# Optimization experiments

Hardware: AMD Instinct MI355X
Metric: run time of the kernel (lower is better)

The kernel has to match this reference:

```python
import jax, jax.numpy as jnp
import numpy as np

B, D, S, K = 2048, 256, 64, 1024
TOPK = 3
MAX_REC = 5
BETA = 0.25  # vq_commitment_beta


def setup_inputs() -> dict:
    key = jax.random.key(0)
    ks = jax.random.split(key, 8)
    w_scale = 1.0 / np.sqrt(2 * D)
    return {
        "gw_real": jax.random.normal(ks[0], (B, D), jnp.float32),
        "gw_imag": jax.random.normal(ks[1], (B, D), jnp.float32),
        "mem_real": jax.random.normal(ks[2], (B, S, D), jnp.float32),
        "mem_imag": jax.random.normal(ks[3], (B, S, D), jnp.float32),
        "gate_w": jax.random.normal(ks[4], (1, 2 * D), jnp.float32) * w_scale,
        "gate_b": jnp.zeros((1,), jnp.float32),
        "addr_w": jax.random.normal(ks[5], (S, 2 * D), jnp.float32) * w_scale,
        "addr_b": jnp.zeros((S,), jnp.float32),
        "lnr_w": jnp.ones((D,), jnp.float32),
        "lnr_b": jnp.zeros((D,), jnp.float32),
        "lni_w": jnp.ones((D,), jnp.float32),
        "lni_b": jnp.zeros((D,), jnp.float32),
        "cln_scale": jnp.ones((D,), jnp.float32),
        "cln_shift": jnp.zeros((D,), jnp.float32),
        "codebook": jax.random.normal(ks[6], (K, 2 * D), jnp.float32) * (1.0 / np.sqrt(D)),
    }


def _layernorm(x, w, b, eps=1e-6):
    mu = x.mean(-1, keepdims=True)
    var = ((x - mu) ** 2).mean(-1, keepdims=True)  # biased, like torch LayerNorm
    return (x - mu) / jnp.sqrt(var + eps) * w + b


def _assoc_mem(gr, gi, mr, mi, gate_w, gate_b, addr_w, addr_b, lnr_w, lnr_b, lni_w, lni_b):
    # read: Re(conj(m) * q) summed over dim -> cosine-like similarity [B,S]
    sim = (mr * gr[:, None, :] + mi * gi[:, None, :]).sum(-1)
    sim = sim - jax.lax.stop_gradient(sim.max(-1, keepdims=True))
    attn = jax.nn.softmax(sim, axis=-1)[..., None]  # [B,S,1]
    read_r = (attn * mr).sum(1)
    read_i = (attn * mi).sum(1)
    # write
    flat = jnp.concatenate([gr, gi], -1)  # [B,2D]
    write_gate = jax.nn.sigmoid(flat @ gate_w.T + gate_b)  # [B,1]
    logits = flat @ addr_w.T + addr_b  # [B,S]
    logits = logits - jax.lax.stop_gradient(logits.max(-1, keepdims=True))
    ww = jax.nn.softmax(logits, axis=-1)
    slot_entropy = (-(ww * jnp.log(ww + 1e-10)).sum(-1)).mean()
    top_vals, top_idx = jax.lax.top_k(ww, TOPK)
    sparse = jnp.zeros_like(ww).at[jnp.arange(ww.shape[0])[:, None], top_idx].set(top_vals)
    sparse = sparse / (sparse.sum(-1, keepdims=True) + 1e-6)
    eff = write_gate[:, None, :] * sparse[..., None]  # [B,S,1]
    nmr = (1.0 - eff) * mr + eff * gr[:, None, :]
    nmi = (1.0 - eff) * mi + eff * gi[:, None, :]
    # StableComplexNorm: independent LayerNorm on real / imag
    nmr = _layernorm(nmr, lnr_w, lnr_b)
    nmi = _layernorm(nmi, lni_w, lni_b)
    return read_r, read_i, nmr, nmi, slot_entropy


def _complex_layernorm(zr, zi, scale, shift):
    mag = jnp.sqrt(zr * zr + zi * zi + 1e-8)
    mean = mag.mean(-1, keepdims=True)
    var = jnp.var(jax.lax.stop_gradient(mag), axis=-1, keepdims=True, ddof=1)  # torch .var unbiased
    nm = (mag - mean) / jnp.sqrt(var + 1e-4) * scale + shift
    ang = jax.lax.stop_gradient(jnp.arctan2(zi, zr))
    return nm * jnp.cos(ang), nm * jnp.sin(ang)


def _ema_vq(zr, zi, codebook):
    zf = jnp.concatenate([zr, zi], -1)  # [B,2D]
    x_sq = (zf ** 2).sum(-1, keepdims=True)
    y_sq = (codebook ** 2).sum(-1)
    d = jnp.clip(x_sq + y_sq - 2.0 * zf @ codebook.T, 0.0)
    idx = d.argmin(-1)  # [B]
    zq = codebook[idx]
    loss_sample = BETA * ((jax.lax.stop_gradient(zq) - zf) ** 2).mean(-1)
    zq = zf + jax.lax.stop_gradient(zq - zf)  # straight-through
    probs = jnp.zeros((K,), zf.dtype).at[idx].add(1.0) / zf.shape[0]
    norm_entropy = -(probs * jnp.log(probs + 1e-10)).sum() / np.log(K)
    return zq[..., :D], zq[..., D:], loss_sample, norm_entropy


def reference(gw_real, gw_imag, mem_real, mem_imag, gate_w, gate_b, addr_w, addr_b,
              lnr_w, lnr_b, lni_w, lni_b, cln_scale, cln_shift, codebook):
    gr, gi = gw_real, gw_imag
    mr, mi = mem_real, mem_imag
    aux = jnp.float32(0.0)
    for _ in range(MAX_REC):  # adaptive-halting recursion, fixed depth
        read_r, read_i, mr, mi, slot_ent = _assoc_mem(
            gr, gi, mr, mi, gate_w, gate_b, addr_w, addr_b, lnr_w, lnr_b, lni_w, lni_b)
        cr, ci = _complex_layernorm(gr + read_r, gi + read_i, cln_scale, cln_shift)
        gr, gi, vq_loss, vq_ent = _ema_vq(cr, ci, codebook)
        aux = aux + slot_ent + vq_loss.mean() + vq_ent
    out = jnp.concatenate([gr, gi], -1)  # [B, 2D]
    return out, aux
```

## Files before the change

kernel.cpp:

```cpp
#include <hip/hip_runtime.h>
#include <cstdint>
#include <cstddef>

#define NB 2048
#define ND 256
#define NS 64
#define NK 1024
#define NREC 5
#define BETA 0.25f

template<int CTRL>
__device__ __forceinline__ float dpp_mv(float x){
  union { float f; int i; } u; u.f = x;
  u.i = __builtin_amdgcn_update_dpp(0, u.i, CTRL, 0xF, 0xF, true);
  return u.f;
}
__device__ __forceinline__ float gred_sum16(float v){
  v += dpp_mv<0x128>(v);
  v += dpp_mv<0x124>(v);
  v += dpp_mv<0x122>(v);
  v += dpp_mv<0x121>(v);
  return v;
}
__device__ __forceinline__ float gred_max16(float v){
  v = fmaxf(v, dpp_mv<0x128>(v));
  v = fmaxf(v, dpp_mv<0x124>(v));
  v = fmaxf(v, dpp_mv<0x122>(v));
  v = fmaxf(v, dpp_mv<0x121>(v));
  return v;
}
__device__ __forceinline__ float wred_sum64(float v){
  v = gred_sum16(v);
  v += __shfl_xor(v, 16, 64);
  v += __shfl_xor(v, 32, 64);
  return v;
}
__device__ __forceinline__ float wred_max64(float v){
  v = gred_max16(v);
  v = fmaxf(v, __shfl_xor(v, 16, 64));
  v = fmaxf(v, __shfl_xor(v, 32, 64));
  return v;
}
__device__ __forceinline__ float swz_xor16(float x){
  union { float f; int i; } u; u.f = x;
  u.i = __builtin_amdgcn_ds_swizzle(u.i, 0x401F);
  return u.f;
}

__global__ __launch_bounds__(64) void k_ysq(const float* __restrict__ cb,
                                            float* __restrict__ ysq){
  const int cidx = blockIdx.x;
  const int lanev = threadIdx.x;
  const float4* p = reinterpret_cast<const float4*>(cb + (size_t)cidx * (2*ND) + lanev*8);
  float4 a = p[0], b = p[1];
  float sv = a.x*a.x + a.y*a.y + a.z*a.z + a.w*a.w
           + b.x*b.x + b.y*b.y + b.z*b.z + b.w*b.w;
  sv = wred_sum64(sv);
  if (lanev == 0) ysq[cidx] = sv;
}

__global__ __launch_bounds__(1024) void k_assoc(
    const float* __restrict__ g_r, const float* __restrict__ g_i,
    const float* mem_r_src, const float* mem_i_src,
    float* mem_r_dst, float* mem_i_dst,
    const float* __restrict__ gate_w, const float* __restrict__ gate_b,
    const float* __restrict__ addr_w, const float* __restrict__ addr_b,
    const float* __restrict__ lnr_w, const float* __restrict__ lnr_b,
    const float* __restrict__ lni_w, const float* __restrict__ lni_b,
    const float* __restrict__ cln_s, const float* __restrict__ cln_sh,
    float* __restrict__ zf, float* __restrict__ acc, const int write_mem)
{
  const int t = threadIdx.x;
  const int b = blockIdx.x;
  const int lane = t & 63;
  const int w = t >> 6;
  const int s = t >> 4;
  const int c = t & 15;
  const int d0 = c << 4;

  __shared__ float s_gr[320], s_gi[320];
  __shared__ float s_attn[NS], s_ww[NS], s_eff[NS];
  __shared__ float s_gpart[4], s_p[4], s_q[4];
  __shared__ float s_redA[32*288];
  __shared__ float s_redB[32*288];

  float mr[16], mi[16];
  const size_t base = ((size_t)b*NS + s)*ND + d0;
  {
    const float4* pr = reinterpret_cast<const float4*>(mem_r_src + base);
    const float4* pi = reinterpret_cast<const float4*>(mem_i_src + base);
#pragma unroll
    for (int q = 0; q < 4; q++){
      float4 vr = pr[q], vi = pi[q];
      mr[4*q+0]=vr.x; mr[4*q+1]=vr.y; mr[4*q+2]=vr.z; mr[4*q+3]=vr.w;
      mi[4*q+0]=vi.x; mi[4*q+1]=vi.y; mi[4*q+2]=vi.z; mi[4*q+3]=vi.w;
    }
  }

  if (t < ND){
    float gr = g_r[(size_t)b*ND + t];
    float gi = g_i[(size_t)b*ND + t];
    s_gr[(t>>4)*20 + (t&15)] = gr;
    s_gi[(t>>4)*20 + (t&15)] = gi;
    float gp = gr*gate_w[t] + gi*gate_w[ND + t];
    gp = wred_sum64(gp);
    if (lane == 0) s_gpart[w] = gp;
  }
  if (t < NS) s_eff[t] = 0.f;
  __syncthreads();

  const float4* sgr4 = reinterpret_cast<const float4*>(&s_gr[c*20]);
  const float4* sgi4 = reinterpret_cast<const float4*>(&s_gi[c*20]);

  float gr_[16], gi_[16];
#pragma unroll
  for (int q = 0; q < 4; q++){
    float4 a4 = sgr4[q], b4 = sgi4[q];
    gr_[4*q+0]=a4.x; gr_[4*q+1]=a4.y; gr_[4*q+2]=a4.z; gr_[4*q+3]=a4.w;
    gi_[4*q+0]=b4.x; gi_[4*q+1]=b4.y; gi_[4*q+2]=b4.z; gi_[4*q+3]=b4.w;
  }

  {
    float sp = 0.f;
#pragma unroll
    for (int j = 0; j < 16; j++) sp += mr[j]*gr_[j] + mi[j]*gi_[j];
    sp = gred_sum16(sp);
    if (c == 0) s_attn[s] = sp;
  }
  {
    const float4* awr = reinterpret_cast<const float4*>(addr_w + (size_t)s*(2*ND) + d0);
    const float4* awi = reinterpret_cast<const float4*>(addr_w + (size_t)s*(2*ND) + ND + d0);
    float lp = 0.f;
#pragma unroll
    for (int q = 0; q < 4; q++){
      float4 ar = awr[q], ai = awi[q];
      lp += gr_[4*q+0]*ar.x + gr_[4*q+1]*ar.y + gr_[4*q+2]*ar.z + gr_[4*q+3]*ar.w;
      lp += gi_[4*q+0]*ai.x + gi_[4*q+1]*ai.y + gi_[4*q+2]*ai.z + gi_[4*q+3]*ai.w;
    }
    lp = gred_sum16(lp);
    if (c == 0) s_ww[s] = lp + addr_b[s];
  }
  __syncthreads();

  if (w == 0){
    float v = s_attn[lane];
    float mx = wred_max64(v);
    float p = expf(v - mx);
    float sum = wred_sum64(p);
    s_attn[lane] = p / sum;
  } else if (w == 1){
    float lv = s_ww[lane];
    float lmx = wred_max64(lv);
    float lp = expf(lv - lmx);
    float lsum = wred_sum64(lp);
    float wwv = lp / lsum;
    float es = wred_sum64(-wwv * logf(wwv + 1e-10f));
    if (lane == 0) atomicAdd(&acc[0], es * (1.f/NB));
    float v2 = wwv; const int id0 = lane;
    float tv0=0, tv1=0, tv2=0; int ti0=0, ti1=0, ti2=0;
#pragma unroll
    for (int kk = 0; kk < 3; kk++){
      float bv = v2; int bi = id0;
#pragma unroll
      for (int m = 1; m < 64; m <<= 1){
        float ov = __shfl_xor(bv, m, 64); int oi = __shfl_xor(bi, m, 64);
        if (ov > bv || (ov == bv && oi < bi)){ bv = ov; bi = oi; }
      }
      if (kk == 0){ tv0 = bv; ti0 = bi; }
      else if (kk == 1){ tv1 = bv; ti1 = bi; }
      else { tv2 = bv; ti2 = bi; }
      if (id0 == bi) v2 = -1.f;
    }
    if (lane == 0){
      float wg = 1.f/(1.f + expf(-(s_gpart[0]+s_gpart[1]+s_gpart[2]+s_gpart[3] + gate_b[0])));
      float ssum = tv0 + tv1 + tv2 + 1e-6f;
      s_eff[ti0] = wg * (tv0/ssum);
      s_eff[ti1] = wg * (tv1/ssum);
      s_eff[ti2] = wg * (tv2/ssum);
    }
  }
  __syncthreads();

  const float a_w = s_attn[s];
  {
    const bool wr_ok = ((lane & 31) < 16);
    const int row = 2*w + (lane >> 5);
    float* dstA = &s_redA[row*288 + (lane & 15)*18];
    float* dstB = &s_redB[row*288 + (lane & 15)*18];
#pragma unroll
    for (int j = 0; j < 16; j += 2){
      float x0 = a_w * mr[j],   x1 = a_w * mr[j+1];
      float y0 = x0 + swz_xor16(x0);
      float y1 = x1 + swz_xor16(x1);
      if (wr_ok) *reinterpret_cast<float2*>(dstA + j) = make_float2(y0, y1);
    }
#pragma unroll
    for (int j = 0; j < 16; j += 2){
      float x0 = a_w * mi[j],   x1 = a_w * mi[j+1];
      float y0 = x0 + swz_xor16(x0);
      float y1 = x1 + swz_xor16(x1);
      if (wr_ok) *reinterpret_cast<float2*>(dstB + j) = make_float2(y0, y1);
    }
  }

  if (write_mem){
    const float effv = s_eff[s];
    const float onem = 1.f - effv;
    {
      float ps = 0.f;
#pragma unroll
      for (int j = 0; j < 16; j++){ mr[j] = onem*mr[j] + effv*gr_[j]; ps += mr[j]; }
      float mu = gred_sum16(ps) * (1.f/ND);
      float vs = 0.f;
#pragma unroll
      for (int j = 0; j < 16; j++){ float d_ = mr[j]-mu; vs += d_*d_; }
      float var = gred_sum16(vs) * (1.f/ND);
      float inv = 1.f / sqrtf(var + 1e-6f);
      const float4* lw4 = reinterpret_cast<const float4*>(lnr_w + d0);
      const float4* lb4 = reinterpret_cast<const float4*>(lnr_b + d0);
#pragma unroll
      for (int q = 0; q < 4; q++){
        float4 wv = lw4[q], bv = lb4[q];
        mr[4*q+0] = (mr[4*q+0]-mu)*inv*wv.x + bv.x;
        mr[4*q+1] = (mr[4*q+1]-mu)*inv*wv.y + bv.y;
        mr[4*q+2] = (mr[4*q+2]-mu)*inv*wv.z + bv.z;
        mr[4*q+3] = (mr[4*q+3]-mu)*inv*wv.w + bv.w;
      }
    }
    {
      float ps = 0.f;
#pragma unroll
      for (int j = 0; j < 16; j++){ mi[j] = onem*mi[j] + effv*gi_[j]; ps += mi[j]; }
      float mu = gred_sum16(ps) * (1.f/ND);
      float vs = 0.f;
#pragma unroll
      for (int j = 0; j < 16; j++){ float d_ = mi[j]-mu; vs += d_*d_; }
      float var = gred_sum16(vs) * (1.f/ND);
      float inv = 1.f / sqrtf(var + 1e-6f);
      const float4* lw4 = reinterpret_cast<const float4*>(lni_w + d0);
      const float4* lb4 = reinterpret_cast<const float4*>(lni_b + d0);
#pragma unroll
      for (int q = 0; q < 4; q++){
        float4 wv = lw4[q], bv = lb4[q];
        mi[4*q+0] = (mi[4*q+0]-mu)*inv*wv.x + bv.x;
        mi[4*q+1] = (mi[4*q+1]-mu)*inv*wv.y + bv.y;
        mi[4*q+2] = (mi[4*q+2]-mu)*inv*wv.z + bv.z;
        mi[4*q+3] = (mi[4*q+3]-mu)*inv*wv.w + bv.w;
      }
    }
  }
  __syncthreads();

  float zr = 0.f, zi = 0.f, mag = 1.f;
  if (t < ND){
    const int offp = (t >> 4)*18 + (t & 15);
    float rr = 0.f, ri = 0.f;
#pragma unroll
    for (int r2 = 0; r2 < 32; r2++){
      rr += s_redA[r2*288 + offp];
      ri += s_redB[r2*288 + offp];
    }
    const int offg = (t >> 4)*20 + (t & 15);
    zr = s_gr[offg] + rr;
    zi = s_gi[offg] + ri;
    mag = sqrtf(zr*zr + zi*zi + 1e-8f);
    float ps = wred_sum64(mag);
    if (lane == 0) s_p[w] = ps;
  }
  __syncthreads();
  const float meanv = (s_p[0]+s_p[1]+s_p[2]+s_p[3]) * (1.f/ND);
  if (t < ND){
    float d_ = mag - meanv;
    float qs = wred_sum64(d_*d_);
    if (lane == 0) s_q[w] = qs;
  }
  __syncthreads();
  if (t < ND){
    const float varv = (s_q[0]+s_q[1]+s_q[2]+s_q[3]) * (1.f/(ND-1));
    float nm = (mag - meanv) / sqrtf(varv + 1e-4f) * cln_s[t] + cln_sh[t];
    float sc = nm / mag;
    zf[(size_t)b*(2*ND) + t]      = sc * zr;
    zf[(size_t)b*(2*ND) + ND + t] = sc * zi;
  }

  if (write_mem){
    float4* pdr = reinterpret_cast<float4*>(mem_r_dst + base);
    float4* pdi = reinterpret_cast<float4*>(mem_i_dst + base);
#pragma unroll
    for (int q = 0; q < 4; q++){
      pdr[q] = make_float4(mr[4*q], mr[4*q+1], mr[4*q+2], mr[4*q+3]);
      pdi[q] = make_float4(mi[4*q], mi[4*q+1], mi[4*q+2], mi[4*q+3]);
    }
  }
}

__global__ __launch_bounds__(256) void k_vq_dist(
    const float* __restrict__ zf, const float* __restrict__ codebook,
    const float* __restrict__ ysq, float* __restrict__ pvals, int* __restrict__ pidx)
{
  const int t = threadIdx.x;
  const int mt = blockIdx.x >> 2, nt = blockIdx.x & 3;
  const int sb = mt*32, cbase = nt*256;
  const int jg = t & 31;
  const int ig = t >> 5;

  __shared__ float s_a[16*36];
  __shared__ float s_b[16*260];

  float accv[4][8];
#pragma unroll
  for (int i = 0; i < 4; i++)
#pragma unroll
    for (int j = 0; j < 8; j++) accv[i][j] = 0.f;

  for (int k0 = 0; k0 < 2*ND; k0 += 16){
#pragma unroll
    for (int p = 0; p < 2; p++){
      int e = t + p*256; int i_ = e >> 4; int k_ = e & 15;
      s_a[k_*36 + i_] = zf[(size_t)(sb+i_)*(2*ND) + k0 + k_];
    }
#pragma unroll
    for (int p = 0; p < 16; p++){
      int e = t + p*256; int c_ = e >> 4; int k_ = e & 15;
      s_b[k_*260 + c_] = codebook[(size_t)(cbase+c_)*(2*ND) + k0 + k_];
    }
    __syncthreads();
#pragma unroll
    for (int k = 0; k < 16; k++){
      float4 a4 = *reinterpret_cast<const float4*>(&s_a[k*36 + ig*4]);
      float4 b0 = *reinterpret_cast<const float4*>(&s_b[k*260 + jg*8]);
      float4 b1 = *reinterpret_cast<const float4*>(&s_b[k*260 + jg*8 + 4]);
      const float av[4] = {a4.x, a4.y, a4.z, a4.w};
      const float bv[8] = {b0.x,b0.y,b0.z,b0.w,b1.x,b1.y,b1.z,b1.w};
#pragma unroll
      for (int i = 0; i < 4; i++)
#pragma unroll
        for (int j = 0; j < 8; j++) accv[i][j] = fmaf(av[i], bv[j], accv[i][j]);
    }
    __syncthreads();
  }

#pragma unroll
  for (int i = 0; i < 4; i++){
    float bvv = 1e30f; int bii = 0;
#pragma unroll
    for (int j = 0; j < 8; j++){
      int cg = cbase + jg*8 + j;
      float sc = ysq[cg] - 2.f*accv[i][j];
      if (sc < bvv){ bvv = sc; bii = cg; }
    }
#pragma unroll
    for (int m = 1; m < 32; m <<= 1){
      float ov = __shfl_xor(bvv, m, 64); int oi = __shfl_xor(bii, m, 64);
      if (ov < bvv || (ov == bvv && oi < bii)){ bvv = ov; bii = oi; }
    }
    if (jg == 0){
      int smp = sb + ig*4 + i;
      pvals[smp*4 + nt] = bvv;
      pidx [smp*4 + nt] = bii;
    }
  }
}

__global__ __launch_bounds__(64) void k_vq_pick(
    const float* __restrict__ pvals, const int* __restrict__ pidx,
    const float* __restrict__ codebook, const float* zf,
    float* __restrict__ g_r, float* __restrict__ g_i, float* out,
    const int final_it, int* __restrict__ hist, float* __restrict__ acc)
{
  const int b = blockIdx.x, lanev = threadIdx.x;
  int sidx = 0;
  if (lanev == 0){
    float bv = pvals[b*4]; int bi = pidx[b*4];
#pragma unroll
    for (int nt = 1; nt < 4; nt++){
      float v = pvals[b*4+nt]; int id = pidx[b*4+nt];
      if (v < bv || (v == bv && id < bi)){ bv = v; bi = id; }
    }
    sidx = bi;
    atomicAdd(&hist[sidx], 1);
  }
  sidx = __shfl(sidx, 0, 64);

  const int e0 = lanev*8;
  const float4* cp = reinterpret_cast<const float4*>(codebook + (size_t)sidx*(2*ND) + e0);
  float4 c0 = cp[0], c1 = cp[1];
  const float4* zp = reinterpret_cast<const float4*>(zf + (size_t)b*(2*ND) + e0);
  float4 z0 = zp[0], z1 = zp[1];
  float ds_ = (c0.x-z0.x)*(c0.x-z0.x) + (c0.y-z0.y)*(c0.y-z0.y)
            + (c0.z-z0.z)*(c0.z-z0.z) + (c0.w-z0.w)*(c0.w-z0.w)
            + (c1.x-z1.x)*(c1.x-z1.x) + (c1.y-z1.y)*(c1.y-z1.y)
            + (c1.z-z1.z)*(c1.z-z1.z) + (c1.w-z1.w)*(c1.w-z1.w);
  ds_ = wred_sum64(ds_);
  if (lanev == 0) atomicAdd(&acc[1], BETA * ds_ * (1.f/(2*ND)) * (1.f/NB));

  if (final_it){
    float4* op = reinterpret_cast<float4*>(out + (size_t)b*(2*ND) + e0);
    op[0] = c0; op[1] = c1;
  } else if (e0 < ND){
    float4* gp = reinterpret_cast<float4*>(g_r + (size_t)b*ND + e0);
    gp[0] = c0; gp[1] = c1;
  } else {
    float4* gp = reinterpret_cast<float4*>(g_i + (size_t)b*ND + (e0-ND));
    gp[0] = c0; gp[1] = c1;
  }
}

__global__ __launch_bounds__(256) void k_final(const int* __restrict__ hist,
                                               const float* __restrict__ acc,
                                               float* __restrict__ out)
{
  __shared__ float red[256];
  const int t = threadIdx.x;
  float e = 0.f;
  for (int it = 0; it < NREC; it++){
    for (int k = t; k < NK; k += 256){
      float p = (float)hist[it*NK + k] * (1.f/NB);
      e += p * logf(p + 1e-10f);
    }
  }
  red[t] = e;
  __syncthreads();
  for (int off = 128; off > 0; off >>= 1){
    if (t < off) red[t] += red[t+off];
    __syncthreads();
  }
  if (t == 0) out[(size_t)NB*2*ND] = acc[0] + acc[1] - red[0] * (1.f/logf((float)NK));
}

extern "C" void kernel_launch(void* const* d_in, const int* in_sizes, int n_in,
                              void* d_out, int out_size, void* d_ws, size_t ws_size,
                              hipStream_t stream)
{
  const float* gwr    = (const float*)d_in[0];
  const float* gwi    = (const float*)d_in[1];
  float*       memr_in= (float*)d_in[2];
  float*       memi_in= (float*)d_in[3];
  const float* gate_w = (const float*)d_in[4];
  const float* gate_b = (const float*)d_in[5];
  const float* addr_w = (const float*)d_in[6];
  const float* addr_b = (const float*)d_in[7];
  const float* lnr_w  = (const float*)d_in[8];
  const float* lnr_b  = (const float*)d_in[9];
  const float* lni_w  = (const float*)d_in[10];
  const float* lni_b  = (const float*)d_in[11];
  const float* cln_s  = (const float*)d_in[12];
  const float* cln_sh = (const float*)d_in[13];
  const float* codebook = (const float*)d_in[14];
  float* out = (float*)d_out;
  char* wsb = (char*)d_ws;

  const size_t OFF_ACC = 0;
  const size_t OFF_HIST = 256;
  const size_t OFF_YSQ = 20736;
  const size_t OFF_PV  = 24832;
  const size_t OFF_PI  = 57600;
  const size_t OFF_GR  = 90368;
  const size_t OFF_GI  = 2187520;
  const size_t OFF_ZF  = 4284672;
  const size_t OFF_MR  = 8478976;
  const size_t OFF_MI  = 142696704;
  const size_t NEED_BIG = 276914432;
  const size_t NEED_MID = 8478976;
  const size_t NEED_TINY = 90368;

  if (ws_size < NEED_TINY) return;

  float* acc   = (float*)(wsb + OFF_ACC);
  int*   hist  = (int*)  (wsb + OFF_HIST);
  float* ysq   = (float*)(wsb + OFF_YSQ);
  float* pvals = (float*)(wsb + OFF_PV);
  int*   pidx  = (int*)  (wsb + OFF_PI);

  const bool big = ws_size >= NEED_BIG;
  const bool mid = ws_size >= NEED_MID;

  float* memr_buf = big ? (float*)(wsb + OFF_MR) : memr_in;
  float* memi_buf = big ? (float*)(wsb + OFF_MI) : memi_in;
  float* g_rp = mid ? (float*)(wsb + OFF_GR) : (float*)d_in[0];
  float* g_ip = mid ? (float*)(wsb + OFF_GI) : (float*)d_in[1];
  float* zfp  = mid ? (float*)(wsb + OFF_ZF) : out;

  (void)hipMemsetAsync(wsb, 0, OFF_HIST + (size_t)NREC*NK*sizeof(int), stream);

  k_ysq<<<dim3(NK), dim3(64), 0, stream>>>(codebook, ysq);

  const float* gsr = gwr; const float* gsi = gwi;
  const float* msr = memr_in; const float* msi = memi_in;
  for (int it = 0; it < NREC; it++){
    const int write_mem = (it == NREC-1) ? 0 : 1;
    k_assoc<<<dim3(NB), dim3(1024), 0, stream>>>(
        gsr, gsi, msr, msi, memr_buf, memi_buf,
        gate_w, gate_b, addr_w, addr_b,
        lnr_w, lnr_b, lni_w, lni_b, cln_s, cln_sh, zfp, acc, write_mem);
    k_vq_dist<<<dim3(256), dim3(256), 0, stream>>>(zfp, codebook, ysq, pvals, pidx);
    k_vq_pick<<<dim3(NB), dim3(64), 0, stream>>>(
        pvals, pidx, codebook, zfp, g_rp, g_ip, out,
        (it == NREC-1) ? 1 : 0, hist + it*NK, acc);
    gsr = g_rp; gsi = g_ip;
    msr = memr_buf; msi = memi_buf;
  }
  k_final<<<dim3(1), dim3(256), 0, stream>>>(hist, acc, out);
}
```

Baseline: 1.588 ms.

## Shrink assoc kernel to 256 threads looping over four slot groups

The associative-memory kernel drops from 1024 to 256 threads per block. Each thread now loops over four groups of 16 memory slots. Because it no longer holds one slot's row in registers across the whole kernel, memory is loaded twice from global, once for similarity and once for the read/write pass. The shared reduction buffers shrink from 32 rows to 4, accumulated across loop iterations, and the layernorm stats use a single pass (sum and sum of squares). The goal is less shared memory, fewer barriers and higher occupancy, at the cost of re-reading memory and a less numerically stable variance.

```diff
diff --git a/kernel.cpp b/kernel.cpp
--- a/kernel.cpp
+++ b/kernel.cpp
@@ -40,11 +40,6 @@
   v = fmaxf(v, __shfl_xor(v, 16, 64));
   v = fmaxf(v, __shfl_xor(v, 32, 64));
   return v;
-}
-__device__ __forceinline__ float swz_xor16(float x){
-  union { float f; int i; } u; u.f = x;
-  u.i = __builtin_amdgcn_ds_swizzle(u.i, 0x401F);
-  return u.f;
 }
 
 __global__ __launch_bounds__(64) void k_ysq(const float* __restrict__ cb,
@@ -59,7 +54,7 @@
   if (lanev == 0) ysq[cidx] = sv;
 }
 
-__global__ __launch_bounds__(1024) void k_assoc(
+__global__ __launch_bounds__(256, 6) void k_assoc(
     const float* __restrict__ g_r, const float* __restrict__ g_i,
     const float* mem_r_src, const float* mem_i_src,
     float* mem_r_dst, float* mem_i_dst,
@@ -74,71 +69,59 @@
   const int b = blockIdx.x;
   const int lane = t & 63;
   const int w = t >> 6;
-  const int s = t >> 4;
+  const int sg = t >> 4;
   const int c = t & 15;
   const int d0 = c << 4;
 
   __shared__ float s_gr[320], s_gi[320];
   __shared__ float s_attn[NS], s_ww[NS], s_eff[NS];
-  __shared__ float s_gpart[4], s_p[4], s_q[4];
-  __shared__ float s_redA[32*288];
-  __shared__ float s_redB[32*288];
-
-  float mr[16], mi[16];
-  const size_t base = ((size_t)b*NS + s)*ND + d0;
+  __shared__ float s_gpart[4], s_pq[8];
+  __shared__ float s_redA[4*288], s_redB[4*288];
+
   {
-    const float4* pr = reinterpret_cast<const float4*>(mem_r_src + base);
-    const float4* pi = reinterpret_cast<const float4*>(mem_i_src + base);
-#pragma unroll
-    for (int q = 0; q < 4; q++){
-      float4 vr = pr[q], vi = pi[q];
-      mr[4*q+0]=vr.x; mr[4*q+1]=vr.y; mr[4*q+2]=vr.z; mr[4*q+3]=vr.w;
-      mi[4*q+0]=vi.x; mi[4*q+1]=vi.y; mi[4*q+2]=vi.z; mi[4*q+3]=vi.w;
-    }
-  }
-
-  if (t < ND){
     float gr = g_r[(size_t)b*ND + t];
     float gi = g_i[(size_t)b*ND + t];
-    s_gr[(t>>4)*20 + (t&15)] = gr;
-    s_gi[(t>>4)*20 + (t&15)] = gi;
+    s_gr[(t>>4)*20 + c] = gr;
+    s_gi[(t>>4)*20 + c] = gi;
+    if (t < NS) s_eff[t] = 0.f;
     float gp = gr*gate_w[t] + gi*gate_w[ND + t];
     gp = wred_sum64(gp);
     if (lane == 0) s_gpart[w] = gp;
   }
-  if (t < NS) s_eff[t] = 0.f;
   __syncthreads();
 
-  const float4* sgr4 = reinterpret_cast<const float4*>(&s_gr[c*20]);
-  const float4* sgi4 = reinterpret_cast<const float4*>(&s_gi[c*20]);
-
   float gr_[16], gi_[16];
-#pragma unroll
-  for (int q = 0; q < 4; q++){
-    float4 a4 = sgr4[q], b4 = sgi4[q];
-    gr_[4*q+0]=a4.x; gr_[4*q+1]=a4.y; gr_[4*q+2]=a4.z; gr_[4*q+3]=a4.w;
-    gi_[4*q+0]=b4.x; gi_[4*q+1]=b4.y; gi_[4*q+2]=b4.z; gi_[4*q+3]=b4.w;
-  }
-
   {
-    float sp = 0.f;
-#pragma unroll
-    for (int j = 0; j < 16; j++) sp += mr[j]*gr_[j] + mi[j]*gi_[j];
+    const float4* p4r = reinterpret_cast<const float4*>(&s_gr[c*20]);
+    const float4* p4i = reinterpret_cast<const float4*>(&s_gi[c*20]);
+#pragma unroll
+    for (int q = 0; q < 4; q++){
+      float4 a4 = p4r[q], b4 = p4i[q];
+      gr_[4*q+0]=a4.x; gr_[4*q+1]=a4.y; gr_[4*q+2]=a4.z; gr_[4*q+3]=a4.w;
+      gi_[4*q+0]=b4.x; gi_[4*q+1]=b4.y; gi_[4*q+2]=b4.z; gi_[4*q+3]=b4.w;
+    }
+  }
+
+#pragma unroll 1
+  for (int p = 0; p < 4; p++){
+    const int sl = (p << 4) + sg;
+    const size_t mbase = ((size_t)b*NS + sl)*ND + d0;
+    const float4* pr  = reinterpret_cast<const float4*>(mem_r_src + mbase);
+    const float4* pi  = reinterpret_cast<const float4*>(mem_i_src + mbase);
+    const float4* ar4 = reinterpret_cast<const float4*>(addr_w + (size_t)sl*(2*ND) + d0);
+    const float4* ai4 = reinterpret_cast<const float4*>(addr_w + (size_t)sl*(2*ND) + ND + d0);
+    float sp = 0.f, lp = 0.f;
+#pragma unroll
+    for (int q = 0; q < 4; q++){
+      float4 vr = pr[q], vi = pi[q], ar = ar4[q], ai = ai4[q];
+      sp += vr.x*gr_[4*q+0] + vr.y*gr_[4*q+1] + vr.z*gr_[4*q+2] + vr.w*gr_[4*q+3];
+      sp += vi.x*gi_[4*q+0] + vi.y*gi_[4*q+1] + vi.z*gi_[4*q+2] + vi.w*gi_[4*q+3];
+      lp += ar.x*gr_[4*q+0] + ar.y*gr_[4*q+1] + ar.z*gr_[4*q+2] + ar.w*gr_[4*q+3];
+      lp += ai.x*gi_[4*q+0] + ai.y*gi_[4*q+1] + ai.z*gi_[4*q+2] + ai.w*gi_[4*q+3];
+    }
     sp = gred_sum16(sp);
-    if (c == 0) s_attn[s] = sp;
-  }
-  {
-    const float4* awr = reinterpret_cast<const float4*>(addr_w + (size_t)s*(2*ND) + d0);
-    const float4* awi = reinterpret_cast<const float4*>(addr_w + (size_t)s*(2*ND) + ND + d0);
-    float lp = 0.f;
-#pragma unroll
-    for (int q = 0; q < 4; q++){
-      float4 ar = awr[q], ai = awi[q];
-      lp += gr_[4*q+0]*ar.x + gr_[4*q+1]*ar.y + gr_[4*q+2]*ar.z + gr_[4*q+3]*ar.w;
-      lp += gi_[4*q+0]*ai.x + gi_[4*q+1]*ai.y + gi_[4*q+2]*ai.z + gi_[4*q+3]*ai.w;
-    }
     lp = gred_sum16(lp);
-    if (c == 0) s_ww[s] = lp + addr_b[s];
+    if (c == 0){ s_attn[sl] = sp; s_ww[sl] = lp + addr_b[sl]; }
   }
   __syncthreads();
 
@@ -178,119 +161,119 @@
       s_eff[ti1] = wg * (tv1/ssum);
       s_eff[ti2] = wg * (tv2/ssum);
     }
+  } else {
+    for (int i = t & 127; i < 4*288; i += 128){ s_redA[i] = 0.f; s_redB[i] = 0.f; }
   }
   __syncthreads();
 
-  const float a_w = s_attn[s];
+#pragma unroll 1
+  for (int p = 0; p < 4; p++){
+    const int sl = (p << 4) + sg;
+    const size_t mbase = ((size_t)b*NS + sl)*ND + d0;
+    float mr[16], mi[16];
+    {
+      const float4* pr = reinterpret_cast<const float4*>(mem_r_src + mbase);
+      const float4* pi = reinterpret_cast<const float4*>(mem_i_src + mbase);
+#pragma unroll
+      for (int q = 0; q < 4; q++){
+        float4 vr = pr[q], vi = pi[q];
+        mr[4*q+0]=vr.x; mr[4*q+1]=vr.y; mr[4*q+2]=vr.z; mr[4*q+3]=vr.w;
+        mi[4*q+0]=vi.x; mi[4*q+1]=vi.y; mi[4*q+2]=vi.z; mi[4*q+3]=vi.w;
+      }
+    }
+    const float a_w = s_attn[sl];
+
+#pragma unroll
+    for (int j = 0; j < 16; j += 2){
+      float y0 = a_w*mr[j], y1 = a_w*mr[j+1];
+      y0 += __shfl_xor(y0, 16, 64); y0 += __shfl_xor(y0, 32, 64);
+      y1 += __shfl_xor(y1, 16, 64); y1 += __shfl_xor(y1, 32, 64);
+      float z0 = a_w*mi[j], z1 = a_w*mi[j+1];
+      z0 += __shfl_xor(z0, 16, 64); z0 += __shfl_xor(z0, 32, 64);
+      z1 += __shfl_xor(z1, 16, 64); z1 += __shfl_xor(z1, 32, 64);
+      if (lane < 16){
+        float2* pa = reinterpret_cast<float2*>(&s_redA[w*288 + lane*18 + j]);
+        float2* pb = reinterpret_cast<float2*>(&s_redB[w*288 + lane*18 + j]);
+        float2 oa = *pa, ob = *pb;
+        *pa = make_float2(oa.x + y0, oa.y + y1);
+        *pb = make_float2(ob.x + z0, ob.y + z1);
+      }
+    }
+
+    if (write_mem){
+      const float effv = s_eff[sl];
+      const float onem = 1.f - effv;
+      {
+        float ps = 0.f;
+#pragma unroll
+        for (int j = 0; j < 16; j++){ mr[j] = onem*mr[j] + effv*gr_[j]; ps += mr[j]; }
+        float mu = gred_sum16(ps) * (1.f/ND);
+        float vs = 0.f;
+#pragma unroll
+        for (int j = 0; j < 16; j++){ float d_ = mr[j]-mu; vs += d_*d_; }
+        float var = gred_sum16(vs) * (1.f/ND);
+        float inv = 1.f / sqrtf(var + 1e-6f);
+        const float4* lw4 = reinterpret_cast<const float4*>(lnr_w + d0);
+        const float4* lb4 = reinterpret_cast<const float4*>(lnr_b + d0);
+        float4* pd = reinterpret_cast<float4*>(mem_r_dst + mbase);
+#pragma unroll
+        for (int q = 0; q < 4; q++){
+          float4 wv = lw4[q], bv = lb4[q];
+          pd[q] = make_float4((mr[4*q+0]-mu)*inv*wv.x + bv.x,
+                              (mr[4*q+1]-mu)*inv*wv.y + bv.y,
+                              (mr[4*q+2]-mu)*inv*wv.z + bv.z,
+                              (mr[4*q+3]-mu)*inv*wv.w + bv.w);
+        }
+      }
+      {
+        float ps = 0.f;
+#pragma unroll
+        for (int j = 0; j < 16; j++){ mi[j] = onem*mi[j] + effv*gi_[j]; ps += mi[j]; }
+        float mu = gred_sum16(ps) * (1.f/ND);
+        float vs = 0.f;
+#pragma unroll
+        for (int j = 0; j < 16; j++){ float d_ = mi[j]-mu; vs += d_*d_; }
+        float var = gred_sum16(vs) * (1.f/ND);
+        float inv = 1.f / sqrtf(var + 1e-6f);
+        const float4* lw4 = reinterpret_cast<const float4*>(lni_w + d0);
+        const float4* lb4 = reinterpret_cast<const float4*>(lni_b + d0);
+        float4* pd = reinterpret_cast<float4*>(mem_i_dst + mbase);
+#pragma unroll
+        for (int q = 0; q < 4; q++){
+          float4 wv = lw4[q], bv = lb4[q];
+          pd[q] = make_float4((mi[4*q+0]-mu)*inv*wv.x + bv.x,
+                              (mi[4*q+1]-mu)*inv*wv.y + bv.y,
+                              (mi[4*q+2]-mu)*inv*wv.z + bv.z,
+                              (mi[4*q+3]-mu)*inv*wv.w + bv.w);
+        }
+      }
+    }
+  }
+  __syncthreads();
+
   {
-    const bool wr_ok = ((lane & 31) < 16);
-    const int row = 2*w + (lane >> 5);
-    float* dstA = &s_redA[row*288 + (lane & 15)*18];
-    float* dstB = &s_redB[row*288 + (lane & 15)*18];
-#pragma unroll
-    for (int j = 0; j < 16; j += 2){
-      float x0 = a_w * mr[j],   x1 = a_w * mr[j+1];
-      float y0 = x0 + swz_xor16(x0);
-      float y1 = x1 + swz_xor16(x1);
-      if (wr_ok) *reinterpret_cast<float2*>(dstA + j) = make_float2(y0, y1);
-    }
-#pragma unroll
-    for (int j = 0; j < 16; j += 2){
-      float x0 = a_w * mi[j],   x1 = a_w * mi[j+1];
-      float y0 = x0 + swz_xor16(x0);
-      float y1 = x1 + swz_xor16(x1);
-      if (wr_ok) *reinterpret_cast<float2*>(dstB + j) = make_float2(y0, y1);
-    }
-  }
-
-  if (write_mem){
-    const float effv = s_eff[s];
-    const float onem = 1.f - effv;
-    {
-      float ps = 0.f;
-#pragma unroll
-      for (int j = 0; j < 16; j++){ mr[j] = onem*mr[j] + effv*gr_[j]; ps += mr[j]; }
-      float mu = gred_sum16(ps) * (1.f/ND);
-      float vs = 0.f;
-#pragma unroll
-      for (int j = 0; j < 16; j++){ float d_ = mr[j]-mu; vs += d_*d_; }
-      float var = gred_sum16(vs) * (1.f/ND);
-      float inv = 1.f / sqrtf(var + 1e-6f);
-      const float4* lw4 = reinterpret_cast<const float4*>(lnr_w + d0);
-      const float4* lb4 = reinterpret_cast<const float4*>(lnr_b + d0);
-#pragma unroll
-      for (int q = 0; q < 4; q++){
-        float4 wv = lw4[q], bv = lb4[q];
-        mr[4*q+0] = (mr[4*q+0]-mu)*inv*wv.x + bv.x;
-        mr[4*q+1] = (mr[4*q+1]-mu)*inv*wv.y + bv.y;
-        mr[4*q+2] = (mr[4*q+2]-mu)*inv*wv.z + bv.z;
-        mr[4*q+3] = (mr[4*q+3]-mu)*inv*wv.w + bv.w;
-      }
-    }
-    {
-      float ps = 0.f;
-#pragma unroll
-      for (int j = 0; j < 16; j++){ mi[j] = onem*mi[j] + effv*gi_[j]; ps += mi[j]; }
-      float mu = gred_sum16(ps) * (1.f/ND);
-      float vs = 0.f;
-#pragma unroll
-      for (int j = 0; j < 16; j++){ float d_ = mi[j]-mu; vs += d_*d_; }
-      float var = gred_sum16(vs) * (1.f/ND);
-      float inv = 1.f / sqrtf(var + 1e-6f);
-      const float4* lw4 = reinterpret_cast<const float4*>(lni_w + d0);
-      const float4* lb4 = reinterpret_cast<const float4*>(lni_b + d0);
-#pragma unroll
-      for (int q = 0; q < 4; q++){
-        float4 wv = lw4[q], bv = lb4[q];
-        mi[4*q+0] = (mi[4*q+0]-mu)*inv*wv.x + bv.x;
-        mi[4*q+1] = (mi[4*q+1]-mu)*inv*wv.y + bv.y;
-        mi[4*q+2] = (mi[4*q+2]-mu)*inv*wv.z + bv.z;
-        mi[4*q+3] = (mi[4*q+3]-mu)*inv*wv.w + bv.w;
-      }
-    }
-  }
-  __syncthreads();
-
-  float zr = 0.f, zi = 0.f, mag = 1.f;
-  if (t < ND){
-    const int offp = (t >> 4)*18 + (t & 15);
+    const int offp = (t >> 4)*18 + c;
     float rr = 0.f, ri = 0.f;
 #pragma unroll
-    for (int r2 = 0; r2 < 32; r2++){
-      rr += s_redA[r2*288 + offp];
-      ri += s_redB[r2*288 + offp];
-    }
-    const int offg = (t >> 4)*20 + (t & 15);
-    zr = s_gr[offg] + rr;
-    zi = s_gi[offg] + ri;
-    mag = sqrtf(zr*zr + zi*zi + 1e-8f);
-    float ps = wred_sum64(mag);
-    if (lane == 0) s_p[w] = ps;
-  }
-  __syncthreads();
-  const float meanv = (s_p[0]+s_p[1]+s_p[2]+s_p[3]) * (1.f/ND);
-  if (t < ND){
-    float d_ = mag - meanv;
-    float qs = wred_sum64(d_*d_);
-    if (lane == 0) s_q[w] = qs;
-  }
-  __syncthreads();
-  if (t < ND){
-    const float varv = (s_q[0]+s_q[1]+s_q[2]+s_q[3]) * (1.f/(ND-1));
+    for (int w2 = 0; w2 < 4; w2++){
+      rr += s_redA[w2*288 + offp];
+      ri += s_redB[w2*288 + offp];
+    }
+    const int offg = (t >> 4)*20 + c;
+    float zr = s_gr[offg] + rr;
+    float zi = s_gi[offg] + ri;
+    float mag = sqrtf(zr*zr + zi*zi + 1e-8f);
+    float s1 = wred_sum64(mag);
+    float s2 = wred_sum64(mag*mag);
+    if (lane == 0){ s_pq[w] = s1; s_pq[4+w] = s2; }
+    __syncthreads();
+    const float meanv = (s_pq[0]+s_pq[1]+s_pq[2]+s_pq[3]) * (1.f/ND);
+    const float sumsq = s_pq[4]+s_pq[5]+s_pq[6]+s_pq[7];
+    const float varv  = (sumsq - (float)ND*meanv*meanv) * (1.f/(ND-1));
     float nm = (mag - meanv) / sqrtf(varv + 1e-4f) * cln_s[t] + cln_sh[t];
     float sc = nm / mag;
     zf[(size_t)b*(2*ND) + t]      = sc * zr;
     zf[(size_t)b*(2*ND) + ND + t] = sc * zi;
-  }
-
-  if (write_mem){
-    float4* pdr = reinterpret_cast<float4*>(mem_r_dst + base);
-    float4* pdi = reinterpret_cast<float4*>(mem_i_dst + base);
-#pragma unroll
-    for (int q = 0; q < 4; q++){
-      pdr[q] = make_float4(mr[4*q], mr[4*q+1], mr[4*q+2], mr[4*q+3]);
-      pdi[q] = make_float4(mi[4*q], mi[4*q+1], mi[4*q+2], mi[4*q+3]);
-    }
   }
 }
 
@@ -489,7 +472,7 @@
   const float* msr = memr_in; const float* msi = memi_in;
   for (int it = 0; it < NREC; it++){
     const int write_mem = (it == NREC-1) ? 0 : 1;
-    k_assoc<<<dim3(NB), dim3(1024), 0, stream>>>(
+    k_assoc<<<dim3(NB), dim3(256), 0, stream>>>(
         gsr, gsi, msr, msi, memr_buf, memi_buf,
         gate_w, gate_b, addr_w, addr_b,
         lnr_w, lnr_b, lni_w, lni_b, cln_s, cln_sh, zfp, acc, write_mem);
```

Result: slower. 1.905 ms (+19.9%).
